# Kernel tuning notes

Hardware: AMD Instinct MI355X
Metric: run time of the kernel (lower is better)

## Reference

```python
import jax, jax.numpy as jnp
import numpy as np

SQ, B, H, D = 2048, 1, 16, 64
HIDDEN = H * D


def setup_inputs() -> dict:
    key = jax.random.key(0)
    kq, kk, kv = jax.random.split(key, 3)
    query_layer = jax.random.normal(kq, (SQ, B, H, D), dtype=jnp.float32)
    key_layer = jax.random.normal(kk, (SQ, B, H, D), dtype=jnp.float32)
    value_layer = jax.random.normal(kv, (SQ, B, H, D), dtype=jnp.float32)
    return {"query_layer": query_layer, "key_layer": key_layer, "value_layer": value_layer}


def reference(query_layer, key_layer, value_layer):
    sq, b, h, d = query_layer.shape
    sk = key_layer.shape[0]
    norm = 1.0 / jnp.sqrt(jnp.asarray(d, dtype=query_layer.dtype))
    # scores: [b, h, sq, sk]  (materialized in the original via baddbmm)
    scores = jnp.einsum('sbhd,tbhd->bhst', query_layer, key_layer) * norm
    # causal mask (tril over [sq, sk]); masked positions -> -10000.0 as in original
    causal = jnp.tril(jnp.ones((sq, sk), dtype=bool))
    scores = jnp.where(causal[None, None], scores, jnp.asarray(-10000.0, scores.dtype))
    probs = jax.nn.softmax(scores, axis=-1)
    # context: [sq, b, h, d] -> [sq, b, hidden]
    ctx = jnp.einsum('bhst,tbhd->sbhd', probs, value_layer)
    return ctx.reshape(sq, b, h * d)
```

## Files before the change

### kernel.cpp

```cpp
#include <hip/hip_runtime.h>

typedef __bf16 bf16_t;
typedef bf16_t bf16x4 __attribute__((ext_vector_type(4)));
typedef bf16_t bf16x8 __attribute__((ext_vector_type(8)));
typedef float f32x4 __attribute__((ext_vector_type(4)));
typedef float f32x16 __attribute__((ext_vector_type(16)));

namespace {
constexpr int kNH  = 16;
constexpr int kHD  = 64;
constexpr int kHID = kNH * kHD;
constexpr int kKP  = 72;
constexpr int oQ = 0;
constexpr int oK = 64 * kKP;
constexpr int kOmPitch = 68;
constexpr int kSmBytes = 35840;
}

__global__ __launch_bounds__(256, 2)
void fattn_kernel(const float* __restrict__ Qg, const float* __restrict__ Kg,
                  const float* __restrict__ Vg, float* __restrict__ Og) {
  __shared__ __align__(16) unsigned char smraw[kSmBytes];
  bf16_t* sm = (bf16_t*)smraw;

  const int bid  = blockIdx.x;
  const int head = bid & (kNH - 1);
  const int idx16 = bid >> 4;
  const int mblk  = (bid < 256) ? (31 - idx16) : (idx16 - 16);
  const int m0   = mblk * 64;
  const int mtk  = 2 * mblk + 1;

  const int tid  = threadIdx.x;
  const int wave = tid >> 6;
  const int lane = tid & 63;
  const int h    = lane >> 5;
  const int m31  = lane & 31;

  bf16_t* qs = sm + oQ;
  bf16_t* ks = sm + oK + wave * 32 * kKP;

  const float kQScale = 0.125f * 1.44269504088896340736f;

  #pragma unroll
  for (int i = 0; i < 4; ++i) {
    const int idx = tid + 256 * i;
    const int row = idx >> 4;
    const int c4  = (idx & 15) * 4;
    const float4 f = *(const float4*)(Qg + (size_t)(m0 + row) * kHID + head * kHD + c4);
    bf16x4 hq;
    hq[0] = (bf16_t)(f.x * kQScale); hq[1] = (bf16_t)(f.y * kQScale);
    hq[2] = (bf16_t)(f.z * kQScale); hq[3] = (bf16_t)(f.w * kQScale);
    *(bf16x4*)(qs + row * kKP + c4) = hq;
  }
  __syncthreads();

  f32x16 Oa00, Oa10, Oa01, Oa11;
  #pragma unroll
  for (int r = 0; r < 16; ++r) { Oa00[r] = 0.f; Oa10[r] = 0.f; Oa01[r] = 0.f; Oa11[r] = 0.f; }
  float lacc0 = 0.f, lacc1 = 0.f;

  const int krow0 = lane >> 4;
  const int kc4   = (lane & 15) * 4;
  const float* kbase = Kg + head * kHD + kc4;
  const float* vbase = Vg + head * kHD + (size_t)(4 * h) * kHID + m31;

  float4 kreg[8];
  float  vv[32];

  if (wave <= mtk) {
    const int kv0 = wave * 32;
    #pragma unroll
    for (int i = 0; i < 8; ++i)
      kreg[i] = *(const float4*)(kbase + (size_t)(kv0 + krow0 + 4 * i) * kHID);
    const float* vt0 = vbase + (size_t)kv0 * kHID;
    #pragma unroll
    for (int db = 0; db < 2; ++db)
      #pragma unroll
      for (int tp = 0; tp < 2; ++tp)
        #pragma unroll
        for (int j = 0; j < 8; ++j)
          vv[db * 16 + tp * 8 + j] =
              vt0[(size_t)(16 * tp + (j & 3) + 8 * (j >> 2)) * kHID + 32 * db];
  }

  for (int jt = wave; jt <= mtk; jt += 4) {
    const int kv0 = jt * 32;

    #pragma unroll
    for (int i = 0; i < 8; ++i) {
      bf16x4 hk;
      hk[0] = (bf16_t)kreg[i].x; hk[1] = (bf16_t)kreg[i].y;
      hk[2] = (bf16_t)kreg[i].z; hk[3] = (bf16_t)kreg[i].w;
      *(bf16x4*)(ks + (krow0 + 4 * i) * kKP + kc4) = hk;
    }

    bf16x8 va0, va1, va2, va3;
    #pragma unroll
    for (int j = 0; j < 8; ++j) {
      va0[j] = (bf16_t)vv[j];
      va1[j] = (bf16_t)vv[8 + j];
      va2[j] = (bf16_t)vv[16 + j];
      va3[j] = (bf16_t)vv[24 + j];
    }

    if (jt + 4 <= mtk) {
      const int kn = (jt + 4) * 32;
      #pragma unroll
      for (int i = 0; i < 8; ++i)
        kreg[i] = *(const float4*)(kbase + (size_t)(kn + krow0 + 4 * i) * kHID);
      const float* vt0 = vbase + (size_t)kn * kHID;
      #pragma unroll
      for (int db = 0; db < 2; ++db)
        #pragma unroll
        for (int tp = 0; tp < 2; ++tp)
          #pragma unroll
          for (int j = 0; j < 8; ++j)
            vv[db * 16 + tp * 8 + j] =
                vt0[(size_t)(16 * tp + (j & 3) + 8 * (j >> 2)) * kHID + 32 * db];
    }

    if (kv0 <= m0) {
      f32x16 cs;
      #pragma unroll
      for (int r = 0; r < 16; ++r) cs[r] = 0.f;
      #pragma unroll
      for (int t = 0; t < 4; ++t) {
        bf16x8 af = *(const bf16x8*)(ks + m31 * kKP + 16 * t + 8 * h);
        bf16x8 qf = *(const bf16x8*)(qs + m31 * kKP + 16 * t + 8 * h);
        cs = __builtin_amdgcn_mfma_f32_32x32x16_bf16(af, qf, cs, 0, 0, 0);
      }
      float p[16];
      if (kv0 == m0) {
        #pragma unroll
        for (int r = 0; r < 16; ++r) {
          const int kr = (r & 3) + 8 * (r >> 2) + 4 * h;
          const float e = __builtin_amdgcn_exp2f(cs[r]);
          p[r] = (kr <= m31) ? e : 0.f;
          lacc0 += p[r];
        }
      } else {
        #pragma unroll
        for (int r = 0; r < 16; ++r) { p[r] = __builtin_amdgcn_exp2f(cs[r]); lacc0 += p[r]; }
      }
      bf16x8 pb0, pb1;
      #pragma unroll
      for (int j = 0; j < 8; ++j) { pb0[j] = (bf16_t)p[j]; pb1[j] = (bf16_t)p[8 + j]; }
      Oa00 = __builtin_amdgcn_mfma_f32_32x32x16_bf16(va0, pb0, Oa00, 0, 0, 0);
      Oa10 = __builtin_amdgcn_mfma_f32_32x32x16_bf16(va2, pb0, Oa10, 0, 0, 0);
      Oa00 = __builtin_amdgcn_mfma_f32_32x32x16_bf16(va1, pb1, Oa00, 0, 0, 0);
      Oa10 = __builtin_amdgcn_mfma_f32_32x32x16_bf16(va3, pb1, Oa10, 0, 0, 0);
    }

    {
      f32x16 cs;
      #pragma unroll
      for (int r = 0; r < 16; ++r) cs[r] = 0.f;
      #pragma unroll
      for (int t = 0; t < 4; ++t) {
        bf16x8 af = *(const bf16x8*)(ks + m31 * kKP + 16 * t + 8 * h);
        bf16x8 qf = *(const bf16x8*)(qs + (32 + m31) * kKP + 16 * t + 8 * h);
        cs = __builtin_amdgcn_mfma_f32_32x32x16_bf16(af, qf, cs, 0, 0, 0);
      }
      float p[16];
      if (kv0 == m0 + 32) {
        #pragma unroll
        for (int r = 0; r < 16; ++r) {
          const int kr = (r & 3) + 8 * (r >> 2) + 4 * h;
          const float e = __builtin_amdgcn_exp2f(cs[r]);
          p[r] = (kr <= m31) ? e : 0.f;
          lacc1 += p[r];
        }
      } else {
        #pragma unroll
        for (int r = 0; r < 16; ++r) { p[r] = __builtin_amdgcn_exp2f(cs[r]); lacc1 += p[r]; }
      }
      bf16x8 pb0, pb1;
      #pragma unroll
      for (int j = 0; j < 8; ++j) { pb0[j] = (bf16_t)p[j]; pb1[j] = (bf16_t)p[8 + j]; }
      Oa01 = __builtin_amdgcn_mfma_f32_32x32x16_bf16(va0, pb0, Oa01, 0, 0, 0);
      Oa11 = __builtin_amdgcn_mfma_f32_32x32x16_bf16(va2, pb0, Oa11, 0, 0, 0);
      Oa01 = __builtin_amdgcn_mfma_f32_32x32x16_bf16(va1, pb1, Oa01, 0, 0, 0);
      Oa11 = __builtin_amdgcn_mfma_f32_32x32x16_bf16(va3, pb1, Oa11, 0, 0, 0);
    }
  }

  float* fv   = (float*)smraw;
  float* Om   = fv + wave * 32 * kOmPitch;
  float* larr = fv + 4 * 32 * kOmPitch;

  #pragma unroll
  for (int qh = 0; qh < 2; ++qh) {
    __syncthreads();
    {
      const f32x16& A0 = qh ? Oa01 : Oa00;
      const f32x16& A1 = qh ? Oa11 : Oa10;
      #pragma unroll
      for (int q = 0; q < 4; ++q) {
        f32x4 v0, v1;
        #pragma unroll
        for (int e = 0; e < 4; ++e) { v0[e] = A0[4 * q + e]; v1[e] = A1[4 * q + e]; }
        *(f32x4*)(Om + (size_t)m31 * kOmPitch + 8 * q + 4 * h)      = v0;
        *(f32x4*)(Om + (size_t)m31 * kOmPitch + 32 + 8 * q + 4 * h) = v1;
      }
      larr[wave * 64 + lane] = qh ? lacc1 : lacc0;
    }
    __syncthreads();
    #pragma unroll
    for (int i = 0; i < 2; ++i) {
      const int idx = tid + 256 * i;
      const int row = idx >> 4;
      const int c4  = (idx & 15) * 4;
      float l = 0.f;
      #pragma unroll
      for (int w = 0; w < 4; ++w)
        l += larr[w * 64 + row] + larr[w * 64 + 32 + row];
      const float inv = 1.f / l;
      f32x4 o;
      #pragma unroll
      for (int e = 0; e < 4; ++e) o[e] = 0.f;
      #pragma unroll
      for (int w = 0; w < 4; ++w) {
        const f32x4 a = *(const f32x4*)(fv + w * 32 * kOmPitch + (size_t)row * kOmPitch + c4);
        #pragma unroll
        for (int e = 0; e < 4; ++e) o[e] += a[e];
      }
      #pragma unroll
      for (int e = 0; e < 4; ++e) o[e] *= inv;
      *(f32x4*)(Og + (size_t)(m0 + 32 * qh + row) * kHID + head * kHD + c4) = o;
    }
  }
}

extern "C" void kernel_launch(void* const* d_in, const int* in_sizes, int n_in,
                              void* d_out, int out_size, void* d_ws, size_t ws_size,
                              hipStream_t stream) {
  (void)in_sizes; (void)n_in; (void)d_ws; (void)ws_size; (void)out_size;
  const float* Q = (const float*)d_in[0];
  const float* K = (const float*)d_in[1];
  const float* V = (const float*)d_in[2];
  float* O = (float*)d_out;
  dim3 grid(512);
  dim3 block(256);
  hipLaunchKernelGGL(fattn_kernel, grid, block, 0, stream, Q, K, V, O);
}
```

Measured before the change: 92.35 us.

## Pre-convert K and V to bf16 in MFMA-friendly layout via prep kernel

Adds a separate prep kernel that converts K and V from fp32 to bf16 in a workspace buffer. K is stored head-major and V is pre-permuted into the per-lane MFMA operand order. The attention kernel then loads 16-byte bf16 vectors instead of strided fp32 scalars, which halves the bytes each block re-reads and removes the per-tile conversions. The cost is an extra kernel launch plus a full read and write of K and V before attention starts.

```diff
diff --git a/kernel.cpp b/kernel.cpp
--- a/kernel.cpp
+++ b/kernel.cpp
@@ -10,16 +10,54 @@
 constexpr int kNH  = 16;
 constexpr int kHD  = 64;
 constexpr int kHID = kNH * kHD;
+constexpr int kSQ  = 2048;
 constexpr int kKP  = 72;
 constexpr int oQ = 0;
 constexpr int oK = 64 * kKP;
 constexpr int kOmPitch = 68;
 constexpr int kSmBytes = 35840;
+constexpr int kKbElems = kNH * kSQ * kHD;
+}
+
+__global__ __launch_bounds__(256)
+void prep_kernel(const float* __restrict__ Kg, const float* __restrict__ Vg,
+                 bf16_t* __restrict__ Kb, bf16_t* __restrict__ Vb) {
+  const int bid = blockIdx.x;
+  const int tid = threadIdx.x;
+  if (bid < 1024) {
+    const int o    = (bid * 256 + tid) * 8;
+    const int head = o >> 17;
+    const int t    = (o >> 6) & 2047;
+    const int d0   = o & 63;
+    const float4 f0 = *(const float4*)(Kg + (size_t)t * kHID + head * kHD + d0);
+    const float4 f1 = *(const float4*)(Kg + (size_t)t * kHID + head * kHD + d0 + 4);
+    bf16x8 hk;
+    hk[0] = (bf16_t)f0.x; hk[1] = (bf16_t)f0.y; hk[2] = (bf16_t)f0.z; hk[3] = (bf16_t)f0.w;
+    hk[4] = (bf16_t)f1.x; hk[5] = (bf16_t)f1.y; hk[6] = (bf16_t)f1.z; hk[7] = (bf16_t)f1.w;
+    *(bf16x8*)(Kb + o) = hk;
+  } else {
+    const int vb   = bid - 1024;
+    const int head = vb >> 6;
+    const int tile = vb & 63;
+    const int lane = tid >> 2;
+    const int hh   = lane >> 5;
+    const int m31  = lane & 31;
+    const int q    = tid & 3;
+    const int db   = q >> 1, tp = q & 1;
+    const int tb   = tile * 32 + 4 * hh + 16 * tp;
+    const int d    = m31 + 32 * db;
+    const float* src = Vg + (size_t)tb * kHID + head * kHD + d;
+    bf16x8 hv;
+    #pragma unroll
+    for (int j = 0; j < 8; ++j)
+      hv[j] = (bf16_t)src[(size_t)((j & 3) + 8 * (j >> 2)) * kHID];
+    *(bf16x8*)(Vb + ((size_t)(head * 64 + tile) * 64 + lane) * 32 + (db * 16 + tp * 8)) = hv;
+  }
 }
 
 __global__ __launch_bounds__(256, 2)
-void fattn_kernel(const float* __restrict__ Qg, const float* __restrict__ Kg,
-                  const float* __restrict__ Vg, float* __restrict__ Og) {
+void fattn_kernel(const float* __restrict__ Qg, const bf16_t* __restrict__ Kb,
+                  const bf16_t* __restrict__ Vb, float* __restrict__ Og) {
   __shared__ __align__(16) unsigned char smraw[kSmBytes];
   bf16_t* sm = (bf16_t*)smraw;
 
@@ -59,64 +97,40 @@
   for (int r = 0; r < 16; ++r) { Oa00[r] = 0.f; Oa10[r] = 0.f; Oa01[r] = 0.f; Oa11[r] = 0.f; }
   float lacc0 = 0.f, lacc1 = 0.f;
 
-  const int krow0 = lane >> 4;
-  const int kc4   = (lane & 15) * 4;
-  const float* kbase = Kg + head * kHD + kc4;
-  const float* vbase = Vg + head * kHD + (size_t)(4 * h) * kHID + m31;
-
-  float4 kreg[8];
-  float  vv[32];
+  const int krow = lane >> 1;
+  const int kcol = (lane & 1) * 32;
+  const bf16_t* kbase = Kb + (size_t)head * (kSQ * kHD) + (size_t)krow * kHD + kcol;
+  const bf16_t* vbase = Vb + ((size_t)head * 64 * 64 + lane) * 32;
+
+  bf16x8 kreg[4];
+  bf16x8 vreg[4];
 
   if (wave <= mtk) {
-    const int kv0 = wave * 32;
-    #pragma unroll
-    for (int i = 0; i < 8; ++i)
-      kreg[i] = *(const float4*)(kbase + (size_t)(kv0 + krow0 + 4 * i) * kHID);
-    const float* vt0 = vbase + (size_t)kv0 * kHID;
-    #pragma unroll
-    for (int db = 0; db < 2; ++db)
-      #pragma unroll
-      for (int tp = 0; tp < 2; ++tp)
-        #pragma unroll
-        for (int j = 0; j < 8; ++j)
-          vv[db * 16 + tp * 8 + j] =
-              vt0[(size_t)(16 * tp + (j & 3) + 8 * (j >> 2)) * kHID + 32 * db];
+    #pragma unroll
+    for (int i = 0; i < 4; ++i)
+      kreg[i] = *(const bf16x8*)(kbase + (size_t)(wave * 32) * kHD + 8 * i);
+    #pragma unroll
+    for (int i = 0; i < 4; ++i)
+      vreg[i] = *(const bf16x8*)(vbase + (size_t)wave * 2048 + 8 * i);
   }
 
   for (int jt = wave; jt <= mtk; jt += 4) {
     const int kv0 = jt * 32;
 
     #pragma unroll
-    for (int i = 0; i < 8; ++i) {
-      bf16x4 hk;
-      hk[0] = (bf16_t)kreg[i].x; hk[1] = (bf16_t)kreg[i].y;
-      hk[2] = (bf16_t)kreg[i].z; hk[3] = (bf16_t)kreg[i].w;
-      *(bf16x4*)(ks + (krow0 + 4 * i) * kKP + kc4) = hk;
-    }
-
-    bf16x8 va0, va1, va2, va3;
-    #pragma unroll
-    for (int j = 0; j < 8; ++j) {
-      va0[j] = (bf16_t)vv[j];
-      va1[j] = (bf16_t)vv[8 + j];
-      va2[j] = (bf16_t)vv[16 + j];
-      va3[j] = (bf16_t)vv[24 + j];
-    }
+    for (int i = 0; i < 4; ++i)
+      *(bf16x8*)(ks + krow * kKP + kcol + 8 * i) = kreg[i];
+
+    bf16x8 va0 = vreg[0], va1 = vreg[1], va2 = vreg[2], va3 = vreg[3];
 
     if (jt + 4 <= mtk) {
       const int kn = (jt + 4) * 32;
       #pragma unroll
-      for (int i = 0; i < 8; ++i)
-        kreg[i] = *(const float4*)(kbase + (size_t)(kn + krow0 + 4 * i) * kHID);
-      const float* vt0 = vbase + (size_t)kn * kHID;
-      #pragma unroll
-      for (int db = 0; db < 2; ++db)
-        #pragma unroll
-        for (int tp = 0; tp < 2; ++tp)
-          #pragma unroll
-          for (int j = 0; j < 8; ++j)
-            vv[db * 16 + tp * 8 + j] =
-                vt0[(size_t)(16 * tp + (j & 3) + 8 * (j >> 2)) * kHID + 32 * db];
+      for (int i = 0; i < 4; ++i)
+        kreg[i] = *(const bf16x8*)(kbase + (size_t)kn * kHD + 8 * i);
+      #pragma unroll
+      for (int i = 0; i < 4; ++i)
+        vreg[i] = *(const bf16x8*)(vbase + (size_t)(jt + 4) * 2048 + 8 * i);
     }
 
     if (kv0 <= m0) {
@@ -234,12 +248,15 @@
 extern "C" void kernel_launch(void* const* d_in, const int* in_sizes, int n_in,
                               void* d_out, int out_size, void* d_ws, size_t ws_size,
                               hipStream_t stream) {
-  (void)in_sizes; (void)n_in; (void)d_ws; (void)ws_size; (void)out_size;
+  (void)in_sizes; (void)n_in; (void)ws_size; (void)out_size;
   const float* Q = (const float*)d_in[0];
   const float* K = (const float*)d_in[1];
   const float* V = (const float*)d_in[2];
   float* O = (float*)d_out;
+  bf16_t* Kb = (bf16_t*)d_ws;
+  bf16_t* Vb = Kb + kKbElems;
+  hipLaunchKernelGGL(prep_kernel, dim3(2048), dim3(256), 0, stream, K, V, Kb, Vb);
   dim3 grid(512);
   dim3 block(256);
-  hipLaunchKernelGGL(fattn_kernel, grid, block, 0, stream, Q, K, V, O);
-}
+  hipLaunchKernelGGL(fattn_kernel, grid, block, 0, stream, Q, Kb, Vb, O);
+}
```

New measurement: 89.56 us. 1.03x faster.
